# Kernel optimization log

Measured on AMD Instinct MI355X. Metric: run time of the kernel, lower is better.

Reference implementation:

```python
import jax, jax.numpy as jnp
import numpy as np

N, D, K = 500000, 128, 16

def _glorot(key, shape):
    lim = np.sqrt(6.0 / (shape[0] + shape[-1]))
    return jax.random.uniform(key, shape, jnp.float32, -lim, lim)

def setup_inputs() -> dict:
    key = jax.random.key(0)
    k1, k2, kV, kW, kU = jax.random.split(key, 5)
    x1 = jax.random.normal(k1, (N, D), jnp.float32)
    x2 = jax.random.normal(k2, (1, D), jnp.float32)
    V = _glorot(kV, (K, 2 * D))
    W = _glorot(kW, (K, D, D))
    b = jnp.zeros((K,), jnp.float32)
    U = _glorot(kU, (K, 1))
    return {"x1": x1, "x2": x2, "V": V, "W": W, "b": b, "U": U}

def reference(x1, x2, V, W, b, U):
    # V-term: concat([x1, tile(x2)]) @ V[i]^T, vectorized over K by splitting V.
    d = x1.shape[1]
    v_term = x1 @ V[:, :d].T + x2 @ V[:, d:].T            # (N,K) + (1,K)
    # W-term: (x1 @ W[i]) @ x2^T for each i == x1 @ (W @ x2)^T, vectorized.
    wx2 = jnp.einsum('kde,e->kd', W, x2[0])               # (K,D)
    w_term = x1 @ wx2.T                                   # (N,K)
    out = jax.nn.relu(v_term + w_term + b)                # (N,K)
    return out @ U                                        # (N,1)
```

## Files before the change

kernel.cpp:

```cpp
#include <hip/hip_runtime.h>
#include <hip/hip_bf16.h>


#define D 128
#define KK 16
#define TPB 256
#define CHUNK 32
#define NCHUNK (D / CHUNK)

__global__ void ntn_prep(const float* __restrict__ x2,
                         const float* __restrict__ V,
                         const float* __restrict__ W,
                         const float* __restrict__ b,
                         float* __restrict__ M,
                         float* __restrict__ c) {
    int k = blockIdx.x;
    int d = threadIdx.x;
    __shared__ float x2s[D];
    __shared__ float red[D];
    x2s[d] = x2[d];
    __syncthreads();

    const float* Wrow = W + ((size_t)k * D + d) * D;
    float s = 0.f;
#pragma unroll 8
    for (int e = 0; e < D; ++e) s = fmaf(Wrow[e], x2s[e], s);
    M[k * D + d] = V[k * 2 * D + d] + s;

    red[d] = V[k * 2 * D + D + d] * x2s[d];
    __syncthreads();
    for (int off = D / 2; off > 0; off >>= 1) {
        if (d < off) red[d] += red[d + off];
        __syncthreads();
    }
    if (d == 0) c[k] = red[0] + b[k];
}

__global__ __launch_bounds__(TPB) void ntn_main(const float* __restrict__ x1,
                                                const float* __restrict__ M,
                                                const float* __restrict__ c,
                                                const float* __restrict__ U,
                                                float* __restrict__ out,
                                                int N) {
    __shared__ float xt[TPB][CHUNK + 1];

    const int t = threadIdx.x;
    const int row0 = blockIdx.x * TPB;

    float acc[KK];
#pragma unroll
    for (int k = 0; k < KK; ++k) acc[k] = 0.f;

    const float4* __restrict__ src = (const float4*)x1;

    for (int ch = 0; ch < NCHUNK; ++ch) {
#pragma unroll
        for (int i = 0; i < 8; ++i) {
            int f = i * TPB + t;
            int r = f >> 3;
            int jj = f & 7;
            int grow = row0 + r;
            float4 v = make_float4(0.f, 0.f, 0.f, 0.f);
            if (grow < N) v = src[grow * 32 + ch * 8 + jj];
            xt[r][jj * 4 + 0] = v.x;
            xt[r][jj * 4 + 1] = v.y;
            xt[r][jj * 4 + 2] = v.z;
            xt[r][jj * 4 + 3] = v.w;
        }
        __syncthreads();

        float xr[CHUNK];
#pragma unroll
        for (int j = 0; j < CHUNK; ++j) xr[j] = xt[t][j];

        const float* __restrict__ Mc = M + ch * CHUNK;
#pragma unroll
        for (int k = 0; k < KK; ++k) {
            float a = acc[k];
            const float* __restrict__ Mk = Mc + k * D;
#pragma unroll
            for (int j = 0; j < CHUNK; ++j) a = fmaf(xr[j], Mk[j], a);
            acc[k] = a;
        }
        __syncthreads();
    }

    const int row = row0 + t;
    if (row < N) {
        float s = 0.f;
#pragma unroll
        for (int k = 0; k < KK; ++k)
            s = fmaf(U[k], fmaxf(acc[k] + c[k], 0.f), s);
        out[row] = s;
    }
}

extern "C" void kernel_launch(void* const* d_in, const int* in_sizes, int n_in,
                              void* d_out, int out_size, void* d_ws, size_t ws_size,
                              hipStream_t stream) {
    const float* x1 = (const float*)d_in[0];
    const float* x2 = (const float*)d_in[1];
    const float* V  = (const float*)d_in[2];
    const float* W  = (const float*)d_in[3];
    const float* b  = (const float*)d_in[4];
    const float* U  = (const float*)d_in[5];
    float* out = (float*)d_out;

    float* M = (float*)d_ws;
    float* c = M + KK * D;

    const int N = in_sizes[0] / D;

    ntn_prep<<<KK, D, 0, stream>>>(x2, V, W, b, M, c);

    int grid = (N + TPB - 1) / TPB;
    ntn_main<<<grid, TPB, 0, stream>>>(x1, M, c, U, out, N);
}
```

Before: 370.3 us.

## Split rows across 8 lanes with direct float4 loads and permuted LDS weights

The main kernel no longer stages x1 through a shared-memory transpose. Each group of 8 lanes now reads one row directly with float4 loads, and partial dot products are reduced with xor shuffles. The M matrix is copied into LDS in a permuted layout so each lane reads its float4 weight slices with few bank conflicts, and c and U are kept in registers. The prep kernel is also parallelised so each dot product runs on one wave with a shuffle reduction, in place of 16 blocks doing serial loops. The cost is 8-way redundant epilogue work per row and more shuffles.

New measurement: 423.8 us. 14.4% more time.

```diff
diff --git a/kernel.cpp b/kernel.cpp
--- a/kernel.cpp
+++ b/kernel.cpp
@@ -4,94 +4,114 @@
 
 #define D 128
 #define KK 16
-#define TPB 256
-#define CHUNK 32
-#define NCHUNK (D / CHUNK)
 
-__global__ void ntn_prep(const float* __restrict__ x2,
-                         const float* __restrict__ V,
-                         const float* __restrict__ W,
-                         const float* __restrict__ b,
-                         float* __restrict__ M,
-                         float* __restrict__ c) {
-    int k = blockIdx.x;
-    int d = threadIdx.x;
-    __shared__ float x2s[D];
-    __shared__ float red[D];
-    x2s[d] = x2[d];
-    __syncthreads();
+__global__ __launch_bounds__(256) void ntn_prep(const float* __restrict__ x2,
+                                                const float* __restrict__ V,
+                                                const float* __restrict__ W,
+                                                const float* __restrict__ b,
+                                                float* __restrict__ M,
+                                                float* __restrict__ c) {
+    const int gtid = blockIdx.x * 256 + threadIdx.x;
+    const int wave = gtid >> 6;
+    const int lane = gtid & 63;
+    if (wave >= KK * D + KK) return;
 
-    const float* Wrow = W + ((size_t)k * D + d) * D;
-    float s = 0.f;
-#pragma unroll 8
-    for (int e = 0; e < D; ++e) s = fmaf(Wrow[e], x2s[e], s);
-    M[k * D + d] = V[k * 2 * D + d] + s;
+    float p;
+    if (wave < KK * D) {
+        const int k = wave >> 7, d = wave & (D - 1);
+        const float* Wr = W + ((size_t)(k * D + d)) * D;
+        p = Wr[lane] * x2[lane] + Wr[lane + 64] * x2[lane + 64];
+    } else {
+        const int k = wave - KK * D;
+        const float* Vr = V + (size_t)k * 2 * D + D;
+        p = Vr[lane] * x2[lane] + Vr[lane + 64] * x2[lane + 64];
+    }
+#pragma unroll
+    for (int m = 32; m; m >>= 1) p += __shfl_xor(p, m);
 
-    red[d] = V[k * 2 * D + D + d] * x2s[d];
-    __syncthreads();
-    for (int off = D / 2; off > 0; off >>= 1) {
-        if (d < off) red[d] += red[d + off];
-        __syncthreads();
+    if (lane == 0) {
+        if (wave < KK * D) {
+            const int k = wave >> 7, d = wave & (D - 1);
+            M[wave] = V[(size_t)k * 2 * D + d] + p;
+        } else {
+            const int k = wave - KK * D;
+            c[k] = p + b[k];
+        }
     }
-    if (d == 0) c[k] = red[0] + b[k];
 }
 
-__global__ __launch_bounds__(TPB) void ntn_main(const float* __restrict__ x1,
-                                                const float* __restrict__ M,
+__global__ __launch_bounds__(256) void ntn_main(const float* __restrict__ x1,
+                                                const float* __restrict__ Mg,
                                                 const float* __restrict__ c,
                                                 const float* __restrict__ U,
                                                 float* __restrict__ out,
                                                 int N) {
-    __shared__ float xt[TPB][CHUNK + 1];
+    __shared__ float Ml[KK * D];
 
     const int t = threadIdx.x;
-    const int row0 = blockIdx.x * TPB;
+#pragma unroll
+    for (int i = 0; i < 8; ++i) {
+        int idx = i * 256 + t;
+        int k = idx >> 7, col = idx & (D - 1);
+        int g = col >> 4, q = (col >> 2) & 3, m = col & 3;
+        Ml[k * D + q * 32 + g * 4 + m] = Mg[idx];
+    }
+    __syncthreads();
 
-    float acc[KK];
+    float cu_c[KK], cu_u[KK];
 #pragma unroll
-    for (int k = 0; k < KK; ++k) acc[k] = 0.f;
+    for (int k = 0; k < KK; ++k) { cu_c[k] = c[k]; cu_u[k] = U[k]; }
 
-    const float4* __restrict__ src = (const float4*)x1;
+    const int w = t >> 6;
+    const int l = t & 63;
+    const int g = l & 7;
+    const int r = l >> 3;
+    const int row0 = blockIdx.x * 256 + w * 64;
 
-    for (int ch = 0; ch < NCHUNK; ++ch) {
-#pragma unroll
-        for (int i = 0; i < 8; ++i) {
-            int f = i * TPB + t;
-            int r = f >> 3;
-            int jj = f & 7;
-            int grow = row0 + r;
-            float4 v = make_float4(0.f, 0.f, 0.f, 0.f);
-            if (grow < N) v = src[grow * 32 + ch * 8 + jj];
-            xt[r][jj * 4 + 0] = v.x;
-            xt[r][jj * 4 + 1] = v.y;
-            xt[r][jj * 4 + 2] = v.z;
-            xt[r][jj * 4 + 3] = v.w;
+    for (int it = 0; it < 8; ++it) {
+        const int row = row0 + it * 8 + r;
+
+        float4 xa, xb, xc, xd;
+        if (row < N) {
+            const float4* xp = (const float4*)(x1 + (size_t)row * D + g * 16);
+            xa = xp[0]; xb = xp[1]; xc = xp[2]; xd = xp[3];
+        } else {
+            xa = xb = xc = xd = make_float4(0.f, 0.f, 0.f, 0.f);
         }
-        __syncthreads();
 
-        float xr[CHUNK];
-#pragma unroll
-        for (int j = 0; j < CHUNK; ++j) xr[j] = xt[t][j];
-
-        const float* __restrict__ Mc = M + ch * CHUNK;
+        float acc[KK];
 #pragma unroll
         for (int k = 0; k < KK; ++k) {
-            float a = acc[k];
-            const float* __restrict__ Mk = Mc + k * D;
-#pragma unroll
-            for (int j = 0; j < CHUNK; ++j) a = fmaf(xr[j], Mk[j], a);
+            const float4* mrow = (const float4*)(Ml + k * D) + g;
+            float4 m0 = mrow[0];
+            float4 m1 = mrow[8];
+            float4 m2 = mrow[16];
+            float4 m3 = mrow[24];
+            float a = 0.f;
+            a = fmaf(xa.x, m0.x, a); a = fmaf(xa.y, m0.y, a);
+            a = fmaf(xa.z, m0.z, a); a = fmaf(xa.w, m0.w, a);
+            a = fmaf(xb.x, m1.x, a); a = fmaf(xb.y, m1.y, a);
+            a = fmaf(xb.z, m1.z, a); a = fmaf(xb.w, m1.w, a);
+            a = fmaf(xc.x, m2.x, a); a = fmaf(xc.y, m2.y, a);
+            a = fmaf(xc.z, m2.z, a); a = fmaf(xc.w, m2.w, a);
+            a = fmaf(xd.x, m3.x, a); a = fmaf(xd.y, m3.y, a);
+            a = fmaf(xd.z, m3.z, a); a = fmaf(xd.w, m3.w, a);
             acc[k] = a;
         }
-        __syncthreads();
-    }
 
-    const int row = row0 + t;
-    if (row < N) {
+#pragma unroll
+        for (int k = 0; k < KK; ++k) {
+            acc[k] += __shfl_xor(acc[k], 1);
+            acc[k] += __shfl_xor(acc[k], 2);
+            acc[k] += __shfl_xor(acc[k], 4);
+        }
+
         float s = 0.f;
 #pragma unroll
         for (int k = 0; k < KK; ++k)
-            s = fmaf(U[k], fmaxf(acc[k] + c[k], 0.f), s);
-        out[row] = s;
+            s = fmaf(cu_u[k], fmaxf(acc[k] + cu_c[k], 0.f), s);
+
+        if (g == 0 && row < N) out[row] = s;
     }
 }
 
@@ -111,8 +131,8 @@
 
     const int N = in_sizes[0] / D;
 
-    ntn_prep<<<KK, D, 0, stream>>>(x2, V, W, b, M, c);
+    ntn_prep<<<516, 256, 0, stream>>>(x2, V, W, b, M, c);
 
-    int grid = (N + TPB - 1) / TPB;
-    ntn_main<<<grid, TPB, 0, stream>>>(x1, M, c, U, out, N);
+    int grid = (N + 255) / 256;
+    ntn_main<<<grid, 256, 0, stream>>>(x1, M, c, U, out, N);
 }
```
